# Performance work log

Measured on AMD Instinct MI355X. Metric: run time of the kernel, lower is better.

The kernel has to match this reference:

```python
import jax, jax.numpy as jnp
import numpy as np

N = 100000      # nodes
E = 1600000     # edges (before self-loops)
NFEAT = 256
NHID = 16
HEADS = 8
NCLASS = 16
NEG_SLOPE = 0.2  # PyG GATConv default


def setup_inputs() -> dict:
    key = jax.random.key(0)
    ks = jax.random.split(key, 11)
    s = 0.1
    return {
        "x": jax.random.normal(ks[0], (N, NFEAT), jnp.float32),
        "edge_index": jax.random.randint(ks[1], (2, E), 0, N, jnp.int32),
        # layer 1 params (lin_src weight [H*C, F], att [H, C], bias [H*C])
        "W1": jax.random.normal(ks[2], (HEADS * NHID, NFEAT), jnp.float32) * s,
        "att_src1": jax.random.normal(ks[3], (HEADS, NHID), jnp.float32) * s,
        "att_dst1": jax.random.normal(ks[4], (HEADS, NHID), jnp.float32) * s,
        "b1": jax.random.normal(ks[5], (HEADS * NHID,), jnp.float32) * s,
        # layer 2 params (heads=1, concat=False)
        "W2": jax.random.normal(ks[6], (NCLASS, HEADS * NHID), jnp.float32) * s,
        "att_src2": jax.random.normal(ks[7], (1, NCLASS), jnp.float32) * s,
        "att_dst2": jax.random.normal(ks[8], (1, NCLASS), jnp.float32) * s,
        "b2": jax.random.normal(ks[9], (NCLASS,), jnp.float32) * s,
    }


def _gat_conv(x, src, dst, W, att_src, att_dst, bias, heads, outc, concat):
    """PyG GATConv (eval mode, edge_attr=None, self-loops already in src/dst)."""
    n = x.shape[0]
    h = (x @ W.T).reshape(n, heads, outc)                 # [N, H, C]
    a_src = (h * att_src[None]).sum(-1)                   # [N, H]
    a_dst = (h * att_dst[None]).sum(-1)                   # [N, H]
    alpha = a_src[src] + a_dst[dst]                       # [Etot, H]
    alpha = jax.nn.leaky_relu(alpha, NEG_SLOPE)
    # segment softmax over edges grouped by destination node
    amax = jax.ops.segment_max(alpha, dst, num_segments=n)  # [N, H]
    ex = jnp.exp(alpha - amax[dst])
    denom = jax.ops.segment_sum(ex, dst, num_segments=n)    # [N, H]
    attn = ex / (denom[dst] + 1e-16)                         # [Etot, H]
    msg = h[src] * attn[:, :, None]                          # [Etot, H, C]
    out = jax.ops.segment_sum(msg, dst, num_segments=n)      # [N, H, C]
    out = out.reshape(n, heads * outc) if concat else out.mean(axis=1)
    return out + bias


def reference(x, edge_index, W1, att_src1, att_dst1, b1, W2, att_src2, att_dst2, b2):
    n = x.shape[0]
    loops = jnp.arange(n, dtype=edge_index.dtype)
    src = jnp.concatenate([edge_index[0], loops])  # add_self_loops=True
    dst = jnp.concatenate([edge_index[1], loops])
    h = _gat_conv(x, src, dst, W1, att_src1, att_dst1, b1, HEADS, NHID, True)
    h = jax.nn.elu(h)
    out = _gat_conv(h, src, dst, W2, att_src2, att_dst2, b2, 1, NCLASS, False)
    return jax.nn.log_softmax(out, axis=1)
```

## Files before the change

kernel.cpp:

```cpp
#include <hip/hip_runtime.h>
#include <hip/hip_bf16.h>
#include <stdint.h>

constexpr int N     = 100000;
constexpr int E     = 1600000;
constexpr int ETOT  = E + N;
constexpr int F     = 256;
constexpr int H     = 8;
constexpr int C     = 16;
constexpr int HC    = H * C;
constexpr int NCLS  = 16;
constexpr float NEG_SLOPE = 0.2f;

constexpr int BSHIFT = 8;
constexpr int NBUCK  = (N + 255) >> BSHIFT;
constexpr int BCAP   = 8192;
constexpr int TILE   = 16384;
constexpr int NTILE  = (ETOT + TILE - 1) / TILE;

typedef __attribute__((ext_vector_type(8))) short short8;
typedef __attribute__((ext_vector_type(4))) float f32x4;
typedef __attribute__((ext_vector_type(2))) float f32x2;
typedef __attribute__((ext_vector_type(4))) unsigned int u32x4;

__device__ inline unsigned short f2bf(float f) {
    union { float f; unsigned int u; } v{f};
    unsigned int r = v.u + 0x7FFF + ((v.u >> 16) & 1);
    return (unsigned short)(r >> 16);
}
__device__ inline float bf2f(unsigned short s) {
    union { unsigned int u; float f; } v{(unsigned int)s << 16};
    return v.f;
}
__device__ inline unsigned char f2fp8(float v) {
    return (unsigned char)(__builtin_amdgcn_cvt_pk_fp8_f32(v, v, 0, false) & 0xff);
}


__global__ __launch_bounds__(256) void k_bhist(const int* __restrict__ ei,
                                               int* __restrict__ bcnt) {
    __shared__ int h[NBUCK];
    for (int i = threadIdx.x; i < NBUCK; i += 256) h[i] = 0;
    __syncthreads();
    int t0 = blockIdx.x * TILE;
    int t1 = (t0 + TILE < ETOT) ? t0 + TILE : ETOT;
    for (int e = t0 + threadIdx.x; e < t1; e += 256) {
        int d = (e < E) ? ei[E + e] : (e - E);
        atomicAdd(&h[d >> BSHIFT], 1);
    }
    __syncthreads();
    for (int i = threadIdx.x; i < NBUCK; i += 256) {
        int c = h[i];
        if (c) atomicAdd(&bcnt[i], c);
    }
}

__global__ void k_bscan(const int* __restrict__ bcnt, int* __restrict__ boff,
                        int* __restrict__ bcur, int* __restrict__ off) {
    __shared__ int s[512];
    int tid = threadIdx.x;
    int v = (tid < NBUCK) ? bcnt[tid] : 0;
    s[tid] = v; __syncthreads();
    for (int ofs = 1; ofs < 512; ofs <<= 1) {
        int t = (tid >= ofs) ? s[tid - ofs] : 0;
        __syncthreads();
        s[tid] += t;
        __syncthreads();
    }
    if (tid < NBUCK) { int ex = s[tid] - v; boff[tid] = ex; bcur[tid] = ex; }
    if (tid == 0) off[N] = ETOT;
}

__global__ __launch_bounds__(256) void k_part(const int* __restrict__ ei,
                                              int* __restrict__ bcur,
                                              unsigned int* __restrict__ pairs) {
    __shared__ int h[NBUCK];
    __shared__ int base[NBUCK];
    int t0 = blockIdx.x * TILE;
    int t1 = (t0 + TILE < ETOT) ? t0 + TILE : ETOT;
    for (int i = threadIdx.x; i < NBUCK; i += 256) h[i] = 0;
    __syncthreads();
    for (int e = t0 + threadIdx.x; e < t1; e += 256) {
        int d = (e < E) ? ei[E + e] : (e - E);
        atomicAdd(&h[d >> BSHIFT], 1);
    }
    __syncthreads();
    for (int i = threadIdx.x; i < NBUCK; i += 256) {
        int c = h[i];
        base[i] = c ? atomicAdd(&bcur[i], c) : 0;
    }
    __syncthreads();
    for (int i = threadIdx.x; i < NBUCK; i += 256) h[i] = 0;
    __syncthreads();
    for (int e = t0 + threadIdx.x; e < t1; e += 256) {
        int s, d;
        if (e < E) { s = ei[e]; d = ei[E + e]; } else { s = e - E; d = s; }
        int b = d >> BSHIFT;
        int r = atomicAdd(&h[b], 1);
        pairs[base[b] + r] = ((unsigned)s << 8) | (unsigned)(d & 255);
    }
}

__global__ __launch_bounds__(256) void k_bsort(const unsigned int* __restrict__ pairs,
                                               const int* __restrict__ bcnt,
                                               const int* __restrict__ boff,
                                               int* __restrict__ csr,
                                               int* __restrict__ off) {
    __shared__ int srcs[BCAP];
    __shared__ int csrs[BCAP];
    __shared__ unsigned char dl[BCAP];
    __shared__ int hist[256];
    __shared__ int sc[256];
    int b = blockIdx.x;
    int nb = bcnt[b]; if (nb > BCAP) nb = BCAP;
    int base = boff[b];
    int dbase = b << BSHIFT;
    int ndst = (N - dbase < 256) ? (N - dbase) : 256;
    int tid = threadIdx.x;

    for (int i = tid; i < nb; i += 256) {
        unsigned int p = pairs[base + i];
        srcs[i] = (int)(p >> 8);
        dl[i] = (unsigned char)(p & 255);
    }
    hist[tid] = 0;
    __syncthreads();
    for (int i = tid; i < nb; i += 256) atomicAdd(&hist[dl[i]], 1);
    __syncthreads();
    int v = hist[tid];
    sc[tid] = v;
    __syncthreads();
    for (int ofs = 1; ofs < 256; ofs <<= 1) {
        int t = (tid >= ofs) ? sc[tid - ofs] : 0;
        __syncthreads();
        sc[tid] += t;
        __syncthreads();
    }
    int lo = sc[tid] - v;
    if (tid < ndst) off[dbase + tid] = base + lo;
    hist[tid] = lo;
    __syncthreads();
    for (int i = tid; i < nb; i += 256) {
        int r = atomicAdd(&hist[dl[i]], 1);
        csrs[r] = srcs[i];
    }
    __syncthreads();
    for (int i = tid; i < nb; i += 256) csr[base + i] = csrs[i];
}


__global__ void k_w1cast(const float* __restrict__ W1, unsigned short* __restrict__ w1x) {
    int i = blockIdx.x * 256 + threadIdx.x;
    if (i < HC * F) w1x[i] = f2bf(W1[i]);
}

__global__ void k_wext(const float* __restrict__ W1,
                       const float* __restrict__ aws, const float* __restrict__ awd,
                       unsigned short* __restrict__ w1x) {
    int r = blockIdx.x;
    int k = threadIdx.x;
    int h = r & 7;
    const float* aw = (r < 8) ? aws : awd;
    float acc = 0.f;
#pragma unroll
    for (int c = 0; c < 16; ++c)
        acc += aw[h * 16 + c] * W1[(size_t)(h * 16 + c) * F + k];
    w1x[(size_t)(128 + r) * F + k] = f2bf(acc);
}


__global__ __launch_bounds__(256) void k_gemm1(const float* __restrict__ x,
                                               const unsigned short* __restrict__ w1x,
                                               unsigned char* __restrict__ h1f,
                                               float* __restrict__ as1,
                                               float* __restrict__ ad1) {
    __shared__ unsigned short Ws[HC * F];
    for (int i = threadIdx.x; i < 4096; i += 256) {
        int row = i >> 5;
        int c16 = i & 31;
        u32x4 v = ((const u32x4*)w1x)[i];
        int byte = row * 512 + ((c16 * 16) ^ ((row & 7) << 4));
        *((u32x4*)((char*)Ws + byte)) = v;
    }
    __syncthreads();

    int wid = threadIdx.x >> 6, lane = threadIdx.x & 63;
    int r16 = lane & 15, g = lane >> 4;
    int m = blockIdx.x * 64 + wid * 16 + r16;
    int mc = (m < N) ? m : (N - 1);
    const float* xr = x + (size_t)mc * F;
    const unsigned short* wext = w1x + (size_t)(128 + r16) * F;

    f32x4 acc[9];
#pragma unroll
    for (int nf = 0; nf < 9; ++nf) acc[nf] = (f32x4){0.f, 0.f, 0.f, 0.f};

#pragma unroll
    for (int kk = 0; kk < 8; ++kk) {
        f32x4 a0 = *((const f32x4*)(xr + kk * 32 + g * 8));
        f32x4 a1 = *((const f32x4*)(xr + kk * 32 + g * 8 + 4));
        short8 af;
#pragma unroll
        for (int j = 0; j < 4; ++j) {
            af[j]     = (short)f2bf(a0[j]);
            af[4 + j] = (short)f2bf(a1[j]);
        }
        int kbyte = kk * 64 + g * 16;
#pragma unroll
        for (int nf = 0; nf < 8; ++nf) {
            int row = nf * 16 + r16;
            int byte = row * 512 + (kbyte ^ ((row & 7) << 4));
            short8 bf = *((const short8*)((const char*)Ws + byte));
            acc[nf] = __builtin_amdgcn_mfma_f32_16x16x32_bf16(af, bf, acc[nf], 0, 0, 0);
        }
        short8 bfx = *((const short8*)(wext + kk * 32 + g * 8));
        acc[8] = __builtin_amdgcn_mfma_f32_16x16x32_bf16(af, bfx, acc[8], 0, 0, 0);
    }

    int orow = blockIdx.x * 64 + wid * 16 + g * 4;
#pragma unroll
    for (int j = 0; j < 4; ++j) {
        int rr = orow + j;
        if (rr >= N) continue;
        unsigned char* dst = h1f + (size_t)rr * HC + r16;
#pragma unroll
        for (int nf = 0; nf < 8; ++nf) dst[nf * 16] = f2fp8(acc[nf][j]);
        float v = acc[8][j];
        if (r16 < 8) as1[rr * 8 + r16] = v;
        else         ad1[rr * 8 + (r16 - 8)] = v;
    }
}


__global__ __launch_bounds__(256) void k_agg1(const int* __restrict__ off,
                                              const int* __restrict__ csr,
                                              const unsigned int* __restrict__ h1w,
                                              const float* __restrict__ as1,
                                              const float* __restrict__ ad1,
                                              const float* __restrict__ b1,
                                              const float* __restrict__ W2,
                                              const float* __restrict__ aw_s2,
                                              const float* __restrict__ aw_d2,
                                              unsigned short* __restrict__ h2b,
                                              float* __restrict__ as2,
                                              float* __restrict__ ad2) {
    __shared__ float W2s[128 * 17];
    for (int i = threadIdx.x; i < HC * NCLS; i += 256) {
        int j = i >> 7, k = i & 127;
        int c8 = k >> 3, q = k & 7;
        W2s[(q * 16 + c8) * 17 + j] = W2[i];
    }
    __syncthreads();

    int w = threadIdx.x >> 6, l = threadIdx.x & 63;
    int n = blockIdx.x * 4 + w;
    if (n >= N) return;
    int g  = l >> 4;
    int c8 = l & 15;
    int hh = c8 >> 1;
    unsigned int wb = (unsigned int)(c8 * 2);
    int e0 = off[n], e1 = off[n + 1];
    int deg = e1 - e0;
    float adst = ad1[n * 8 + hh];
    float den = 0.f;
    float acc[8] = {0.f, 0.f, 0.f, 0.f, 0.f, 0.f, 0.f, 0.f};

    int eb = 0;
    for (; eb + 8 <= deg; eb += 8) {
        int sA = csr[e0 + eb + g];
        int sB = csr[e0 + eb + 4 + g];
        float avA = as1[sA * 8 + hh];
        float avB = as1[sB * 8 + hh];
        uint2 vA = *((const uint2*)(h1w + ((unsigned int)sA << 5) + wb));
        uint2 vB = *((const uint2*)(h1w + ((unsigned int)sB << 5) + wb));
        float aA = avA + adst; aA = fmaxf(aA, aA * NEG_SLOPE);
        float aB = avB + adst; aB = fmaxf(aB, aB * NEG_SLOPE);
        float wA = __expf(aA), wB = __expf(aB);
        den += wA + wB;
        f32x2 a01 = __builtin_amdgcn_cvt_pk_f32_fp8(vA.x, false);
        f32x2 a23 = __builtin_amdgcn_cvt_pk_f32_fp8(vA.x, true);
        f32x2 a45 = __builtin_amdgcn_cvt_pk_f32_fp8(vA.y, false);
        f32x2 a67 = __builtin_amdgcn_cvt_pk_f32_fp8(vA.y, true);
        f32x2 b01 = __builtin_amdgcn_cvt_pk_f32_fp8(vB.x, false);
        f32x2 b23 = __builtin_amdgcn_cvt_pk_f32_fp8(vB.x, true);
        f32x2 b45 = __builtin_amdgcn_cvt_pk_f32_fp8(vB.y, false);
        f32x2 b67 = __builtin_amdgcn_cvt_pk_f32_fp8(vB.y, true);
        acc[0] += wA * a01[0] + wB * b01[0];
        acc[1] += wA * a01[1] + wB * b01[1];
        acc[2] += wA * a23[0] + wB * b23[0];
        acc[3] += wA * a23[1] + wB * b23[1];
        acc[4] += wA * a45[0] + wB * b45[0];
        acc[5] += wA * a45[1] + wB * b45[1];
        acc[6] += wA * a67[0] + wB * b67[0];
        acc[7] += wA * a67[1] + wB * b67[1];
    }
    for (; eb < deg; eb += 4) {
        int slot = eb + g;
        bool ok = slot < deg;
        int s = csr[e0 + (ok ? slot : 0)];
        float aval = as1[s * 8 + hh];
        uint2 v = *((const uint2*)(h1w + ((unsigned int)s << 5) + wb));
        float al = aval + adst; al = fmaxf(al, al * NEG_SLOPE);
        float wt = ok ? __expf(al) : 0.f;
        den += wt;
        f32x2 a01 = __builtin_amdgcn_cvt_pk_f32_fp8(v.x, false);
        f32x2 a23 = __builtin_amdgcn_cvt_pk_f32_fp8(v.x, true);
        f32x2 a45 = __builtin_amdgcn_cvt_pk_f32_fp8(v.y, false);
        f32x2 a67 = __builtin_amdgcn_cvt_pk_f32_fp8(v.y, true);
        acc[0] += wt * a01[0];
        acc[1] += wt * a01[1];
        acc[2] += wt * a23[0];
        acc[3] += wt * a23[1];
        acc[4] += wt * a45[0];
        acc[5] += wt * a45[1];
        acc[6] += wt * a67[0];
        acc[7] += wt * a67[1];
    }
#pragma unroll
    for (int q = 0; q < 8; ++q) {
        acc[q] += __shfl_xor(acc[q], 16, 64);
        acc[q] += __shfl_xor(acc[q], 32, 64);
    }
    den += __shfl_xor(den, 16, 64);
    den += __shfl_xor(den, 32, 64);

    float inv = 1.f / (den + 1e-16f);
    float v8[8];
#pragma unroll
    for (int q = 0; q < 8; ++q) {
        float v = acc[q] * inv + b1[c8 * 8 + q];
        v8[q] = (v > 0.f) ? v : (__expf(v) - 1.f);
    }
    float p0 = 0.f, p1 = 0.f, p2 = 0.f, p3 = 0.f;
#pragma unroll
    for (int q = 0; q < 8; ++q) {
        const float* wr = &W2s[(q * 16 + c8) * 17 + g * 4];
        p0 += v8[q] * wr[0];
        p1 += v8[q] * wr[1];
        p2 += v8[q] * wr[2];
        p3 += v8[q] * wr[3];
    }
#pragma unroll
    for (int msk = 8; msk >= 1; msk >>= 1) {
        p0 += __shfl_xor(p0, msk, 64);
        p1 += __shfl_xor(p1, msk, 64);
        p2 += __shfl_xor(p2, msk, 64);
        p3 += __shfl_xor(p3, msk, 64);
    }
    float sa = p0 * aw_s2[g * 4] + p1 * aw_s2[g * 4 + 1]
             + p2 * aw_s2[g * 4 + 2] + p3 * aw_s2[g * 4 + 3];
    float da = p0 * aw_d2[g * 4] + p1 * aw_d2[g * 4 + 1]
             + p2 * aw_d2[g * 4 + 2] + p3 * aw_d2[g * 4 + 3];
    sa += __shfl_xor(sa, 16, 64); sa += __shfl_xor(sa, 32, 64);
    da += __shfl_xor(da, 16, 64); da += __shfl_xor(da, 32, 64);
    if (l == 0) { as2[n] = sa; ad2[n] = da; }
    if (c8 < 4) {
        float h2v = p0;
        h2v = (c8 == 1) ? p1 : h2v;
        h2v = (c8 == 2) ? p2 : h2v;
        h2v = (c8 == 3) ? p3 : h2v;
        h2b[(size_t)n * NCLS + g * 4 + c8] = f2bf(h2v);
    }
}


__global__ __launch_bounds__(256) void k_agg2(const int* __restrict__ off,
                                              const int* __restrict__ csr,
                                              const float* __restrict__ as2,
                                              const float* __restrict__ ad2,
                                              const unsigned short* __restrict__ h2b,
                                              const float* __restrict__ b2,
                                              float* __restrict__ outp) {
    int gpos = threadIdx.x >> 4, c = threadIdx.x & 15;
    int n = blockIdx.x * 16 + gpos;
    if (n >= N) return;
    int e0 = off[n], e1 = off[n + 1];
    float adst = ad2[n];
    float den = 0.f, acc = 0.f;
    int e = e0;
    for (; e + 4 <= e1; e += 4) {
        int s0 = csr[e], s1 = csr[e + 1], s2 = csr[e + 2], s3 = csr[e + 3];
        float x0 = as2[s0], x1 = as2[s1], x2 = as2[s2], x3 = as2[s3];
        unsigned short m0 = h2b[s0 * NCLS + c], m1 = h2b[s1 * NCLS + c];
        unsigned short m2 = h2b[s2 * NCLS + c], m3 = h2b[s3 * NCLS + c];
        float a0 = x0 + adst; a0 = fmaxf(a0, a0 * NEG_SLOPE);
        float a1 = x1 + adst; a1 = fmaxf(a1, a1 * NEG_SLOPE);
        float a2 = x2 + adst; a2 = fmaxf(a2, a2 * NEG_SLOPE);
        float a3 = x3 + adst; a3 = fmaxf(a3, a3 * NEG_SLOPE);
        float w0 = __expf(a0), w1 = __expf(a1), w2 = __expf(a2), w3 = __expf(a3);
        den += (w0 + w1) + (w2 + w3);
        acc += w0 * bf2f(m0) + w1 * bf2f(m1) + w2 * bf2f(m2) + w3 * bf2f(m3);
    }
    for (; e < e1; ++e) {
        int s = csr[e];
        float al = as2[s] + adst;
        al = fmaxf(al, al * NEG_SLOPE);
        float wt = __expf(al);
        den += wt;
        acc += wt * bf2f(h2b[s * NCLS + c]);
    }
    float v = acc / (den + 1e-16f) + b2[c];
    float mx = v;
#pragma unroll
    for (int msk = 8; msk >= 1; msk >>= 1) mx = fmaxf(mx, __shfl_xor(mx, msk, 64));
    float ex = __expf(v - mx), se = ex;
#pragma unroll
    for (int msk = 8; msk >= 1; msk >>= 1) se += __shfl_xor(se, msk, 64);
    outp[n * NCLS + c] = v - mx - __logf(se);
}


extern "C" void kernel_launch(void* const* d_in, const int* in_sizes, int n_in,
                              void* d_out, int out_size, void* d_ws, size_t ws_size,
                              hipStream_t stream) {
    const float* x        = (const float*)d_in[0];
    const int*   ei       = (const int*)d_in[1];
    const float* W1       = (const float*)d_in[2];
    const float* att_src1 = (const float*)d_in[3];
    const float* att_dst1 = (const float*)d_in[4];
    const float* b1       = (const float*)d_in[5];
    const float* W2       = (const float*)d_in[6];
    const float* att_src2 = (const float*)d_in[7];
    const float* att_dst2 = (const float*)d_in[8];
    const float* b2       = (const float*)d_in[9];
    float* outp = (float*)d_out;

    char* p = (char*)d_ws;
    unsigned char* h1f    = (unsigned char*)p;  p += (size_t)N * HC;
    unsigned short* h2b   = (unsigned short*)p; p += (size_t)N * NCLS * 2;
    float* as1  = (float*)p; p += (size_t)N * H * 4;
    float* ad1  = (float*)p; p += (size_t)N * H * 4;
    float* as2  = (float*)p; p += (size_t)N * 4;
    float* ad2  = (float*)p; p += (size_t)N * 4;
    unsigned short* w1x = (unsigned short*)p; p += (size_t)144 * F * 2;
    unsigned int* pairs = (unsigned int*)p; p += (size_t)ETOT * 4;
    int* csr    = (int*)p;   p += (size_t)ETOT * 4;
    int* off    = (int*)p;   p += (size_t)(N + 1) * 4;
    int* bcnt   = (int*)p;   p += (size_t)NBUCK * 4;
    int* boff   = (int*)p;   p += (size_t)NBUCK * 4;
    int* bcur   = (int*)p;   p += (size_t)NBUCK * 4;

    hipMemsetAsync(bcnt, 0, (size_t)NBUCK * 4, stream);

    k_bhist<<<NTILE, 256, 0, stream>>>(ei, bcnt);
    k_bscan<<<1, 512, 0, stream>>>(bcnt, boff, bcur, off);
    k_part<<<NTILE, 256, 0, stream>>>(ei, bcur, pairs);
    k_bsort<<<NBUCK, 256, 0, stream>>>(pairs, bcnt, boff, csr, off);

    k_w1cast<<<(HC * F + 255) / 256, 256, 0, stream>>>(W1, w1x);
    k_wext<<<16, 256, 0, stream>>>(W1, att_src1, att_dst1, w1x);
    k_gemm1<<<(N + 63) / 64, 256, 0, stream>>>(x, w1x, h1f, as1, ad1);
    k_agg1<<<(N + 3) / 4, 256, 0, stream>>>(off, csr, (const unsigned int*)h1f,
                                            as1, ad1, b1, W2, att_src2, att_dst2,
                                            h2b, as2, ad2);

    k_agg2<<<(N + 15) / 16, 256, 0, stream>>>(off, csr, as2, ad2, h2b, b2, outp);
}
```

Measured before the change: 256.9 us.

## Merge independent graph-partition and weight/GEMM kernels into shared launches

Result: faster. 222.4 us (-13.4%).

```diff
diff --git a/kernel.cpp b/kernel.cpp
--- a/kernel.cpp
+++ b/kernel.cpp
@@ -37,21 +37,41 @@
 }
 
 
-__global__ __launch_bounds__(256) void k_bhist(const int* __restrict__ ei,
-                                               int* __restrict__ bcnt) {
+__global__ __launch_bounds__(256) void k_pre(const int* __restrict__ ei,
+                                             int* __restrict__ bcnt,
+                                             const float* __restrict__ W1,
+                                             const float* __restrict__ aws,
+                                             const float* __restrict__ awd,
+                                             unsigned short* __restrict__ w1x) {
     __shared__ int h[NBUCK];
-    for (int i = threadIdx.x; i < NBUCK; i += 256) h[i] = 0;
-    __syncthreads();
-    int t0 = blockIdx.x * TILE;
-    int t1 = (t0 + TILE < ETOT) ? t0 + TILE : ETOT;
-    for (int e = t0 + threadIdx.x; e < t1; e += 256) {
-        int d = (e < E) ? ei[E + e] : (e - E);
-        atomicAdd(&h[d >> BSHIFT], 1);
-    }
-    __syncthreads();
-    for (int i = threadIdx.x; i < NBUCK; i += 256) {
-        int c = h[i];
-        if (c) atomicAdd(&bcnt[i], c);
+    int b = blockIdx.x;
+    if (b < NTILE) {
+        for (int i = threadIdx.x; i < NBUCK; i += 256) h[i] = 0;
+        __syncthreads();
+        int t0 = b * TILE;
+        int t1 = (t0 + TILE < ETOT) ? t0 + TILE : ETOT;
+        for (int e = t0 + threadIdx.x; e < t1; e += 256) {
+            int d = (e < E) ? ei[E + e] : (e - E);
+            atomicAdd(&h[d >> BSHIFT], 1);
+        }
+        __syncthreads();
+        for (int i = threadIdx.x; i < NBUCK; i += 256) {
+            int c = h[i];
+            if (c) atomicAdd(&bcnt[i], c);
+        }
+    } else if (b < NTILE + 128) {
+        int i = (b - NTILE) * 256 + threadIdx.x;
+        if (i < HC * F) w1x[i] = f2bf(W1[i]);
+    } else {
+        int r = b - NTILE - 128;
+        int k = threadIdx.x;
+        int hh = r & 7;
+        const float* aw = (r < 8) ? aws : awd;
+        float acc = 0.f;
+#pragma unroll
+        for (int c = 0; c < 16; ++c)
+            acc += aw[hh * 16 + c] * W1[(size_t)(hh * 16 + c) * F + k];
+        w1x[(size_t)(128 + r) * F + k] = f2bf(acc);
     }
 }
 
@@ -71,33 +91,99 @@
     if (tid == 0) off[N] = ETOT;
 }
 
-__global__ __launch_bounds__(256) void k_part(const int* __restrict__ ei,
-                                              int* __restrict__ bcur,
-                                              unsigned int* __restrict__ pairs) {
-    __shared__ int h[NBUCK];
-    __shared__ int base[NBUCK];
-    int t0 = blockIdx.x * TILE;
-    int t1 = (t0 + TILE < ETOT) ? t0 + TILE : ETOT;
-    for (int i = threadIdx.x; i < NBUCK; i += 256) h[i] = 0;
-    __syncthreads();
-    for (int e = t0 + threadIdx.x; e < t1; e += 256) {
-        int d = (e < E) ? ei[E + e] : (e - E);
-        atomicAdd(&h[d >> BSHIFT], 1);
-    }
-    __syncthreads();
-    for (int i = threadIdx.x; i < NBUCK; i += 256) {
-        int c = h[i];
-        base[i] = c ? atomicAdd(&bcur[i], c) : 0;
-    }
-    __syncthreads();
-    for (int i = threadIdx.x; i < NBUCK; i += 256) h[i] = 0;
-    __syncthreads();
-    for (int e = t0 + threadIdx.x; e < t1; e += 256) {
-        int s, d;
-        if (e < E) { s = ei[e]; d = ei[E + e]; } else { s = e - E; d = s; }
-        int b = d >> BSHIFT;
-        int r = atomicAdd(&h[b], 1);
-        pairs[base[b] + r] = ((unsigned)s << 8) | (unsigned)(d & 255);
+
+__global__ __launch_bounds__(256) void k_mid(const int* __restrict__ ei,
+                                             int* __restrict__ bcur,
+                                             unsigned int* __restrict__ pairs,
+                                             const float* __restrict__ x,
+                                             const unsigned short* __restrict__ w1x,
+                                             unsigned char* __restrict__ h1f,
+                                             float* __restrict__ as1,
+                                             float* __restrict__ ad1) {
+    __shared__ char smem[65536];
+    if (blockIdx.x < NTILE) {
+        int* h    = (int*)smem;
+        int* base = h + NBUCK;
+        int t0 = blockIdx.x * TILE;
+        int t1 = (t0 + TILE < ETOT) ? t0 + TILE : ETOT;
+        for (int i = threadIdx.x; i < NBUCK; i += 256) h[i] = 0;
+        __syncthreads();
+        for (int e = t0 + threadIdx.x; e < t1; e += 256) {
+            int d = (e < E) ? ei[E + e] : (e - E);
+            atomicAdd(&h[d >> BSHIFT], 1);
+        }
+        __syncthreads();
+        for (int i = threadIdx.x; i < NBUCK; i += 256) {
+            int c = h[i];
+            base[i] = c ? atomicAdd(&bcur[i], c) : 0;
+        }
+        __syncthreads();
+        for (int i = threadIdx.x; i < NBUCK; i += 256) h[i] = 0;
+        __syncthreads();
+        for (int e = t0 + threadIdx.x; e < t1; e += 256) {
+            int s, d;
+            if (e < E) { s = ei[e]; d = ei[E + e]; } else { s = e - E; d = s; }
+            int b = d >> BSHIFT;
+            int r = atomicAdd(&h[b], 1);
+            pairs[base[b] + r] = ((unsigned)s << 8) | (unsigned)(d & 255);
+        }
+        return;
+    }
+    unsigned short* Ws = (unsigned short*)smem;
+    int bid = blockIdx.x - NTILE;
+    for (int i = threadIdx.x; i < 4096; i += 256) {
+        int row = i >> 5;
+        int c16 = i & 31;
+        u32x4 v = ((const u32x4*)w1x)[i];
+        int byte = row * 512 + ((c16 * 16) ^ ((row & 7) << 4));
+        *((u32x4*)((char*)Ws + byte)) = v;
+    }
+    __syncthreads();
+
+    int wid = threadIdx.x >> 6, lane = threadIdx.x & 63;
+    int r16 = lane & 15, g = lane >> 4;
+    int m = bid * 64 + wid * 16 + r16;
+    int mc = (m < N) ? m : (N - 1);
+    const float* xr = x + (size_t)mc * F;
+    const unsigned short* wext = w1x + (size_t)(128 + r16) * F;
+
+    f32x4 acc[9];
+#pragma unroll
+    for (int nf = 0; nf < 9; ++nf) acc[nf] = (f32x4){0.f, 0.f, 0.f, 0.f};
+
+#pragma unroll
+    for (int kk = 0; kk < 8; ++kk) {
+        f32x4 a0 = *((const f32x4*)(xr + kk * 32 + g * 8));
+        f32x4 a1 = *((const f32x4*)(xr + kk * 32 + g * 8 + 4));
+        short8 af;
+#pragma unroll
+        for (int j = 0; j < 4; ++j) {
+            af[j]     = (short)f2bf(a0[j]);
+            af[4 + j] = (short)f2bf(a1[j]);
+        }
+        int kbyte = kk * 64 + g * 16;
+#pragma unroll
+        for (int nf = 0; nf < 8; ++nf) {
+            int row = nf * 16 + r16;
+            int byte = row * 512 + (kbyte ^ ((row & 7) << 4));
+            short8 bf = *((const short8*)((const char*)Ws + byte));
+            acc[nf] = __builtin_amdgcn_mfma_f32_16x16x32_bf16(af, bf, acc[nf], 0, 0, 0);
+        }
+        short8 bfx = *((const short8*)(wext + kk * 32 + g * 8));
+        acc[8] = __builtin_amdgcn_mfma_f32_16x16x32_bf16(af, bfx, acc[8], 0, 0, 0);
+    }
+
+    int orow = bid * 64 + wid * 16 + g * 4;
+#pragma unroll
+    for (int j = 0; j < 4; ++j) {
+        int rr = orow + j;
+        if (rr >= N) continue;
+        unsigned char* dst = h1f + (size_t)rr * HC + r16;
+#pragma unroll
+        for (int nf = 0; nf < 8; ++nf) dst[nf * 16] = f2fp8(acc[nf][j]);
+        float v = acc[8][j];
+        if (r16 < 8) as1[rr * 8 + r16] = v;
+        else         ad1[rr * 8 + (r16 - 8)] = v;
     }
 }
 
@@ -146,89 +232,6 @@
     }
     __syncthreads();
     for (int i = tid; i < nb; i += 256) csr[base + i] = csrs[i];
-}
-
-
-__global__ void k_w1cast(const float* __restrict__ W1, unsigned short* __restrict__ w1x) {
-    int i = blockIdx.x * 256 + threadIdx.x;
-    if (i < HC * F) w1x[i] = f2bf(W1[i]);
-}
-
-__global__ void k_wext(const float* __restrict__ W1,
-                       const float* __restrict__ aws, const float* __restrict__ awd,
-                       unsigned short* __restrict__ w1x) {
-    int r = blockIdx.x;
-    int k = threadIdx.x;
-    int h = r & 7;
-    const float* aw = (r < 8) ? aws : awd;
-    float acc = 0.f;
-#pragma unroll
-    for (int c = 0; c < 16; ++c)
-        acc += aw[h * 16 + c] * W1[(size_t)(h * 16 + c) * F + k];
-    w1x[(size_t)(128 + r) * F + k] = f2bf(acc);
-}
-
-
-__global__ __launch_bounds__(256) void k_gemm1(const float* __restrict__ x,
-                                               const unsigned short* __restrict__ w1x,
-                                               unsigned char* __restrict__ h1f,
-                                               float* __restrict__ as1,
-                                               float* __restrict__ ad1) {
-    __shared__ unsigned short Ws[HC * F];
-    for (int i = threadIdx.x; i < 4096; i += 256) {
-        int row = i >> 5;
-        int c16 = i & 31;
-        u32x4 v = ((const u32x4*)w1x)[i];
-        int byte = row * 512 + ((c16 * 16) ^ ((row & 7) << 4));
-        *((u32x4*)((char*)Ws + byte)) = v;
-    }
-    __syncthreads();
-
-    int wid = threadIdx.x >> 6, lane = threadIdx.x & 63;
-    int r16 = lane & 15, g = lane >> 4;
-    int m = blockIdx.x * 64 + wid * 16 + r16;
-    int mc = (m < N) ? m : (N - 1);
-    const float* xr = x + (size_t)mc * F;
-    const unsigned short* wext = w1x + (size_t)(128 + r16) * F;
-
-    f32x4 acc[9];
-#pragma unroll
-    for (int nf = 0; nf < 9; ++nf) acc[nf] = (f32x4){0.f, 0.f, 0.f, 0.f};
-
-#pragma unroll
-    for (int kk = 0; kk < 8; ++kk) {
-        f32x4 a0 = *((const f32x4*)(xr + kk * 32 + g * 8));
-        f32x4 a1 = *((const f32x4*)(xr + kk * 32 + g * 8 + 4));
-        short8 af;
-#pragma unroll
-        for (int j = 0; j < 4; ++j) {
-            af[j]     = (short)f2bf(a0[j]);
-            af[4 + j] = (short)f2bf(a1[j]);
-        }
-        int kbyte = kk * 64 + g * 16;
-#pragma unroll
-        for (int nf = 0; nf < 8; ++nf) {
-            int row = nf * 16 + r16;
-            int byte = row * 512 + (kbyte ^ ((row & 7) << 4));
-            short8 bf = *((const short8*)((const char*)Ws + byte));
-            acc[nf] = __builtin_amdgcn_mfma_f32_16x16x32_bf16(af, bf, acc[nf], 0, 0, 0);
-        }
-        short8 bfx = *((const short8*)(wext + kk * 32 + g * 8));
-        acc[8] = __builtin_amdgcn_mfma_f32_16x16x32_bf16(af, bfx, acc[8], 0, 0, 0);
-    }
-
-    int orow = blockIdx.x * 64 + wid * 16 + g * 4;
-#pragma unroll
-    for (int j = 0; j < 4; ++j) {
-        int rr = orow + j;
-        if (rr >= N) continue;
-        unsigned char* dst = h1f + (size_t)rr * HC + r16;
-#pragma unroll
-        for (int nf = 0; nf < 8; ++nf) dst[nf * 16] = f2fp8(acc[nf][j]);
-        float v = acc[8][j];
-        if (r16 < 8) as1[rr * 8 + r16] = v;
-        else         ad1[rr * 8 + (r16 - 8)] = v;
-    }
 }
 
 
@@ -442,14 +445,12 @@
 
     hipMemsetAsync(bcnt, 0, (size_t)NBUCK * 4, stream);
 
-    k_bhist<<<NTILE, 256, 0, stream>>>(ei, bcnt);
+    k_pre<<<NTILE + 128 + 16, 256, 0, stream>>>(ei, bcnt, W1, att_src1, att_dst1, w1x);
     k_bscan<<<1, 512, 0, stream>>>(bcnt, boff, bcur, off);
-    k_part<<<NTILE, 256, 0, stream>>>(ei, bcur, pairs);
+    k_mid<<<NTILE + (N + 63) / 64, 256, 0, stream>>>(ei, bcur, pairs,
+                                                     x, w1x, h1f, as1, ad1);
     k_bsort<<<NBUCK, 256, 0, stream>>>(pairs, bcnt, boff, csr, off);
 
-    k_w1cast<<<(HC * F + 255) / 256, 256, 0, stream>>>(W1, w1x);
-    k_wext<<<16, 256, 0, stream>>>(W1, att_src1, att_dst1, w1x);
-    k_gemm1<<<(N + 63) / 64, 256, 0, stream>>>(x, w1x, h1f, as1, ad1);
     k_agg1<<<(N + 3) / 4, 256, 0, stream>>>(off, csr, (const unsigned int*)h1f,
                                             as1, ad1, b1, W2, att_src2, att_dst2,
                                             h2b, as2, ad2);
```
